# Kernel tuning notes

Hardware: AMD Instinct MI355X
Metric: run time of the kernel (lower is better)

## Reference

```python
import jax, jax.numpy as jnp
import numpy as np

# TFMBSLinear forward: quantize input and weight to ternary {-1,0,1} via sign,
# compute out = sign(x) @ sign(W)^T (what the ternary fabric T-GEMV kernel
# computes, with zero-skip), then add float bias. The base-3 byte packing is a
# transport encoding only; the math is the ternary matmul.

def setup_inputs() -> dict:
    key = jax.random.key(0)
    k1, k2, k3 = jax.random.split(key, 3)
    B, IN, OUT = 8192, 2048, 2048
    x = jax.random.normal(k1, (B, IN), dtype=jnp.float32)
    # kaiming-uniform-ish init; only sign matters for the fabric kernel
    weight = jax.random.normal(k2, (OUT, IN), dtype=jnp.float32)
    fan_in_bound = 1.0 / np.sqrt(IN)
    bias = jax.random.uniform(k3, (OUT,), dtype=jnp.float32,
                              minval=-fan_in_bound, maxval=fan_in_bound)
    return {"input": x, "weight": weight, "bias": bias}

def reference(input, weight, bias):
    x_t = jnp.sign(input)    # ternary activations [B, IN]
    w_t = jnp.sign(weight)   # ternary weights     [OUT, IN]
    out = jnp.einsum('bi,oi->bo', x_t, w_t)  # T-GEMV accumulation, fp32
    return out + bias
```

## Files before the change

### kernel.cpp

```cpp
#include <hip/hip_runtime.h>


typedef int      intx4    __attribute__((ext_vector_type(4)));
typedef int      intx8    __attribute__((ext_vector_type(8)));
typedef float    floatx16 __attribute__((ext_vector_type(16)));

static constexpr int M = 8192;
static constexpr int N = 2048;
static constexpr int K = 2048;
static constexpr int KB = K / 2;
static constexpr int BM = 256, BN = 128;

__device__ __forceinline__ unsigned nib(float v) {
    unsigned u = __float_as_uint(v);
    return (v != 0.0f) ? (0x2u | ((u >> 28) & 0x8u)) : 0u;
}

__device__ __forceinline__ unsigned pack8(const float4& a, const float4& b) {
    return  nib(a.x)        | (nib(a.y) << 4)  | (nib(a.z) << 8)  | (nib(a.w) << 12)
         | (nib(b.x) << 16) | (nib(b.y) << 20) | (nib(b.z) << 24) | (nib(b.w) << 28);
}

__global__ __launch_bounds__(256) void quant_tile(
    const float* __restrict__ x, const float* __restrict__ w,
    uint4* __restrict__ qx, uint4* __restrict__ qw, int nx, int ntot)
{
    int g = blockIdx.x * 256 + threadIdx.x;
    if (g >= ntot) return;
    const float* src; uint4* dst; int gg;
    if (g < nx) { gg = g; src = x; dst = qx; }
    else        { gg = g - nx; src = w; dst = qw; }
    const int r = gg & 31, h = (gg >> 5) & 1, c = (gg >> 6) & 31, s = gg >> 11;
    const int m = s * 32 + r;
    const float4* p = (const float4*)(src + (size_t)m * K + (c * 2 + h) * 32);
    uint4 o;
    o.x = pack8(p[0], p[1]);
    o.y = pack8(p[2], p[3]);
    o.z = pack8(p[4], p[5]);
    o.w = pack8(p[6], p[7]);
    dst[gg] = o;
}

__device__ __forceinline__ intx8 ext4(intx4 v) {
    return __builtin_shufflevector(v, v, 0, 1, 2, 3, -1, -1, -1, -1);
}

#define MFMA_(A_, B_, C_) __builtin_amdgcn_mfma_scale_f32_32x32x64_f8f6f4( \
    ext4(A_), ext4(B_), C_, 4, 4, 0, 127, 0, 127)

#define GLDS(g_, l_) __builtin_amdgcn_global_load_lds(                      \
    (const __attribute__((address_space(1))) void*)(g_),                    \
    (__attribute__((address_space(3))) void*)(l_), 16, 0, 0)

#define MFMA8()                               \
    acc[0][0] = MFMA_(a0, b0, acc[0][0]);     \
    acc[0][1] = MFMA_(a0, b1, acc[0][1]);     \
    acc[1][0] = MFMA_(a1, b0, acc[1][0]);     \
    acc[1][1] = MFMA_(a1, b1, acc[1][1]);     \
    acc[2][0] = MFMA_(a2, b0, acc[2][0]);     \
    acc[2][1] = MFMA_(a2, b1, acc[2][1]);     \
    acc[3][0] = MFMA_(a3, b0, acc[3][0]);     \
    acc[3][1] = MFMA_(a3, b1, acc[3][1])

#define FRAGS(BUF_, C_)                                                     \
    intx4 a0 = *(const intx4*)(smem + (BUF_) + fAo          + (C_) * 1024); \
    intx4 a1 = *(const intx4*)(smem + (BUF_) + fAo + 2048   + (C_) * 1024); \
    intx4 a2 = *(const intx4*)(smem + (BUF_) + fAo + 4096   + (C_) * 1024); \
    intx4 a3 = *(const intx4*)(smem + (BUF_) + fAo + 6144   + (C_) * 1024); \
    intx4 b0 = *(const intx4*)(smem + (BUF_) + fBo          + (C_) * 1024); \
    intx4 b1 = *(const intx4*)(smem + (BUF_) + fBo + 2048   + (C_) * 1024)

__global__ __launch_bounds__(256, 2) void tgemm_fp4_256x128(
    const char* __restrict__ A,
    const char* __restrict__ B,
    const float* __restrict__ bias,
    float* __restrict__ C)
{
    __shared__ char smem[49152];

    const int tid  = threadIdx.x;
    const int wave = tid >> 6;
    const int lane = tid & 63;
    const int l32  = lane & 31;
    const int half = lane >> 5;

    const int bi    = blockIdx.x;
    const int local = bi >> 3;
    const int bm    = ((bi & 7) * 4 + (local & 3)) * 256;
    const int bn    = (local >> 2) * 128;

    const char* gA0 = A + ((size_t)(bm >> 5) + 2 * wave) * 32768 + lane * 16;
    const char* gA1 = gA0 + 32768;
    const char* gB0 = B + ((size_t)(bn >> 5) + wave) * 32768 + lane * 16;
    const int stA0 = (2 * wave) * 2048;
    const int stA1 = stA0 + 2048;
    const int stB0 = 16384 + wave * 2048;

    const int wm = (wave & 1) * 128;
    const int wn = (wave >> 1) * 64;
    const int fAo = (wm >> 5) * 2048 + lane * 16;
    const int fBo = 16384 + (wn >> 5) * 2048 + lane * 16;

    const int cn0 = bn + wn + l32;
    const float bc0 = bias[cn0];
    const float bc1 = bias[cn0 + 32];

    floatx16 acc[4][2] = {};

    #pragma unroll
    for (int c = 0; c < 2; ++c) {
        GLDS(gA0 + c * 1024, smem + stA0 + c * 1024);
        GLDS(gA1 + c * 1024, smem + stA1 + c * 1024);
        GLDS(gB0 + c * 1024, smem + stB0 + c * 1024);
    }

    #pragma unroll
    for (int t = 0; t < 15; ++t) {
        const int buf  = (t & 1) * 24576;
        const int xbuf = buf ^ 24576;
        #pragma unroll
        for (int c = 0; c < 2; ++c) {
            asm volatile("s_waitcnt vmcnt(3)" ::: "memory");
            __builtin_amdgcn_s_barrier();
            FRAGS(buf, c);
            const int g = (t + 1) * 2 + c;
            GLDS(gA0 + g * 1024, smem + xbuf + stA0 + c * 1024);
            GLDS(gA1 + g * 1024, smem + xbuf + stA1 + c * 1024);
            GLDS(gB0 + g * 1024, smem + xbuf + stB0 + c * 1024);
            __builtin_amdgcn_s_setprio(1);
            MFMA8();
            __builtin_amdgcn_s_setprio(0);
        }
    }

    {
        {
            asm volatile("s_waitcnt vmcnt(3)" ::: "memory");
            __builtin_amdgcn_s_barrier();
            FRAGS(24576, 0);
            __builtin_amdgcn_s_setprio(1);
            MFMA8();
            __builtin_amdgcn_s_setprio(0);
        }
        {
            asm volatile("s_waitcnt vmcnt(0)" ::: "memory");
            __builtin_amdgcn_s_barrier();
            FRAGS(24576, 1);
            __builtin_amdgcn_s_setprio(1);
            MFMA8();
            __builtin_amdgcn_s_setprio(0);
        }
    }

    const int rbase = bm + wm + 4 * half;

    #pragma unroll
    for (int i = 0; i < 4; ++i) {
        #pragma unroll
        for (int r = 0; r < 16; ++r) {
            const int row = rbase + 32 * i + (r & 3) + 8 * (r >> 2);
            __builtin_nontemporal_store(acc[i][0][r] + bc0,
                                        &C[(size_t)row * N + cn0]);
            __builtin_nontemporal_store(acc[i][1][r] + bc1,
                                        &C[(size_t)row * N + cn0 + 32]);
        }
    }
}

extern "C" void kernel_launch(void* const* d_in, const int* in_sizes, int n_in,
                              void* d_out, int out_size, void* d_ws, size_t ws_size,
                              hipStream_t stream) {
    const float* x    = (const float*)d_in[0];
    const float* w    = (const float*)d_in[1];
    const float* bias = (const float*)d_in[2];
    float* out = (float*)d_out;

    char* qx = (char*)d_ws;
    char* qw = qx + (size_t)M * KB;

    const int nx   = (M * KB) / 16;
    const int ntot = nx + (N * KB) / 16;
    quant_tile<<<ntot / 256, 256, 0, stream>>>(
        x, w, (uint4*)qx, (uint4*)qw, nx, ntot);

    tgemm_fp4_256x128<<<dim3((M / BM) * (N / BN)), dim3(256), 0, stream>>>(
        qx, qw, bias, out);
}
```

Before: 144.9 us.

## Load GEMM fragments directly from global memory, dropping LDS staging

Removes the double-buffered global_load_lds staging into shared memory and the per-step barriers. Each wave now reads its MFMA operand fragments straight from the pre-tiled global layout in a simple unrolled loop. The output stores also switch from nontemporal to ordinary stores. This saves LDS traffic and synchronisation, but loses data sharing between waves, since each A/B tile is now fetched twice through cache. It also loses explicit prefetch overlap and leans on L2 hit rates.

```diff
diff --git a/kernel.cpp b/kernel.cpp
--- a/kernel.cpp
+++ b/kernel.cpp
@@ -48,10 +48,6 @@
 #define MFMA_(A_, B_, C_) __builtin_amdgcn_mfma_scale_f32_32x32x64_f8f6f4( \
     ext4(A_), ext4(B_), C_, 4, 4, 0, 127, 0, 127)
 
-#define GLDS(g_, l_) __builtin_amdgcn_global_load_lds(                      \
-    (const __attribute__((address_space(1))) void*)(g_),                    \
-    (__attribute__((address_space(3))) void*)(l_), 16, 0, 0)
-
 #define MFMA8()                               \
     acc[0][0] = MFMA_(a0, b0, acc[0][0]);     \
     acc[0][1] = MFMA_(a0, b1, acc[0][1]);     \
@@ -62,22 +58,12 @@
     acc[3][0] = MFMA_(a3, b0, acc[3][0]);     \
     acc[3][1] = MFMA_(a3, b1, acc[3][1])
 
-#define FRAGS(BUF_, C_)                                                     \
-    intx4 a0 = *(const intx4*)(smem + (BUF_) + fAo          + (C_) * 1024); \
-    intx4 a1 = *(const intx4*)(smem + (BUF_) + fAo + 2048   + (C_) * 1024); \
-    intx4 a2 = *(const intx4*)(smem + (BUF_) + fAo + 4096   + (C_) * 1024); \
-    intx4 a3 = *(const intx4*)(smem + (BUF_) + fAo + 6144   + (C_) * 1024); \
-    intx4 b0 = *(const intx4*)(smem + (BUF_) + fBo          + (C_) * 1024); \
-    intx4 b1 = *(const intx4*)(smem + (BUF_) + fBo + 2048   + (C_) * 1024)
-
-__global__ __launch_bounds__(256, 2) void tgemm_fp4_256x128(
+__global__ __launch_bounds__(256, 2) void tgemm_fp4_direct(
     const char* __restrict__ A,
     const char* __restrict__ B,
     const float* __restrict__ bias,
     float* __restrict__ C)
 {
-    __shared__ char smem[49152];
-
     const int tid  = threadIdx.x;
     const int wave = tid >> 6;
     const int lane = tid & 63;
@@ -89,17 +75,11 @@
     const int bm    = ((bi & 7) * 4 + (local & 3)) * 256;
     const int bn    = (local >> 2) * 128;
 
-    const char* gA0 = A + ((size_t)(bm >> 5) + 2 * wave) * 32768 + lane * 16;
-    const char* gA1 = gA0 + 32768;
-    const char* gB0 = B + ((size_t)(bn >> 5) + wave) * 32768 + lane * 16;
-    const int stA0 = (2 * wave) * 2048;
-    const int stA1 = stA0 + 2048;
-    const int stB0 = 16384 + wave * 2048;
-
     const int wm = (wave & 1) * 128;
     const int wn = (wave >> 1) * 64;
-    const int fAo = (wm >> 5) * 2048 + lane * 16;
-    const int fBo = 16384 + (wn >> 5) * 2048 + lane * 16;
+
+    const char* pA = A + ((size_t)((bm + wm) >> 5)) * 32768 + lane * 16;
+    const char* pB = B + ((size_t)((bn + wn) >> 5)) * 32768 + lane * 16;
 
     const int cn0 = bn + wn + l32;
     const float bc0 = bias[cn0];
@@ -107,49 +87,17 @@
 
     floatx16 acc[4][2] = {};
 
-    #pragma unroll
-    for (int c = 0; c < 2; ++c) {
-        GLDS(gA0 + c * 1024, smem + stA0 + c * 1024);
-        GLDS(gA1 + c * 1024, smem + stA1 + c * 1024);
-        GLDS(gB0 + c * 1024, smem + stB0 + c * 1024);
-    }
-
-    #pragma unroll
-    for (int t = 0; t < 15; ++t) {
-        const int buf  = (t & 1) * 24576;
-        const int xbuf = buf ^ 24576;
-        #pragma unroll
-        for (int c = 0; c < 2; ++c) {
-            asm volatile("s_waitcnt vmcnt(3)" ::: "memory");
-            __builtin_amdgcn_s_barrier();
-            FRAGS(buf, c);
-            const int g = (t + 1) * 2 + c;
-            GLDS(gA0 + g * 1024, smem + xbuf + stA0 + c * 1024);
-            GLDS(gA1 + g * 1024, smem + xbuf + stA1 + c * 1024);
-            GLDS(gB0 + g * 1024, smem + xbuf + stB0 + c * 1024);
-            __builtin_amdgcn_s_setprio(1);
-            MFMA8();
-            __builtin_amdgcn_s_setprio(0);
-        }
-    }
-
-    {
-        {
-            asm volatile("s_waitcnt vmcnt(3)" ::: "memory");
-            __builtin_amdgcn_s_barrier();
-            FRAGS(24576, 0);
-            __builtin_amdgcn_s_setprio(1);
-            MFMA8();
-            __builtin_amdgcn_s_setprio(0);
-        }
-        {
-            asm volatile("s_waitcnt vmcnt(0)" ::: "memory");
-            __builtin_amdgcn_s_barrier();
-            FRAGS(24576, 1);
-            __builtin_amdgcn_s_setprio(1);
-            MFMA8();
-            __builtin_amdgcn_s_setprio(0);
-        }
+    #pragma unroll 4
+    for (int g = 0; g < 32; ++g) {
+        const char* qa = pA + g * 1024;
+        const char* qb = pB + g * 1024;
+        intx4 a0 = *(const intx4*)(qa);
+        intx4 a1 = *(const intx4*)(qa + 32768);
+        intx4 a2 = *(const intx4*)(qa + 65536);
+        intx4 a3 = *(const intx4*)(qa + 98304);
+        intx4 b0 = *(const intx4*)(qb);
+        intx4 b1 = *(const intx4*)(qb + 32768);
+        MFMA8();
     }
 
     const int rbase = bm + wm + 4 * half;
@@ -159,10 +107,8 @@
         #pragma unroll
         for (int r = 0; r < 16; ++r) {
             const int row = rbase + 32 * i + (r & 3) + 8 * (r >> 2);
-            __builtin_nontemporal_store(acc[i][0][r] + bc0,
-                                        &C[(size_t)row * N + cn0]);
-            __builtin_nontemporal_store(acc[i][1][r] + bc1,
-                                        &C[(size_t)row * N + cn0 + 32]);
+            C[(size_t)row * N + cn0]      = acc[i][0][r] + bc0;
+            C[(size_t)row * N + cn0 + 32] = acc[i][1][r] + bc1;
         }
     }
 }
@@ -183,6 +129,6 @@
     quant_tile<<<ntot / 256, 256, 0, stream>>>(
         x, w, (uint4*)qx, (uint4*)qw, nx, ntot);
 
-    tgemm_fp4_256x128<<<dim3((M / BM) * (N / BN)), dim3(256), 0, stream>>>(
+    tgemm_fp4_direct<<<dim3((M / BM) * (N / BN)), dim3(256), 0, stream>>>(
         qx, qw, bias, out);
 }
```

Result: slower. 163.7 us (+13.0%).
